# Kernel optimization log

Hardware: AMD Instinct MI355X
Metric: run time of the kernel (lower is better)

Reference implementation:

```python
import jax, jax.numpy as jnp
import numpy as np
from jax import lax

NUM_HEADS = 8
HEAD_DIM = 32  # filters_per_head


def conv1d_same(x, w, b):
    # x: [B, T, Cin], w: [K, Cin, Cout] (WIO), 'same' padding, stride 1
    y = lax.conv_general_dilated(x, w, window_strides=(1,), padding='SAME',
                                 dimension_numbers=('NWC', 'WIO', 'NWC'))
    return y + b


def setup_inputs() -> dict:
    key = jax.random.key(0)
    ks = jax.random.split(key, 9)
    B, T, C = 8, 2048, 256
    K = 3
    s = 1.0 / np.sqrt(K * C)
    return {
        'x': jax.random.normal(ks[0], (B, T, C), dtype=jnp.float32),
        'Wq': jax.random.normal(ks[1], (K, C, C), dtype=jnp.float32) * s,
        'bq': jnp.zeros((C,), dtype=jnp.float32),
        'Wk': jax.random.normal(ks[2], (K, C, C), dtype=jnp.float32) * s,
        'bk': jnp.zeros((C,), dtype=jnp.float32),
        'Wv': jax.random.normal(ks[3], (K, C, C), dtype=jnp.float32) * s,
        'bv': jnp.zeros((C,), dtype=jnp.float32),
        'Wo': jax.random.normal(ks[4], (K, C, C), dtype=jnp.float32) * s,
        'bo': jnp.zeros((C,), dtype=jnp.float32),
    }


def reference(x, Wq, bq, Wk, bk, Wv, bv, Wo, bo):
    B, T, C = x.shape
    q = conv1d_same(x, Wq, bq)
    k = conv1d_same(x, Wk, bk)
    v = conv1d_same(x, Wv, bv)

    def split(t):  # [B, T, C] -> [B, H, T, D]
        return t.reshape(B, T, NUM_HEADS, HEAD_DIM).transpose(0, 2, 1, 3)

    q, k, v = split(q), split(k), split(v)
    scale = 1.0 / jnp.sqrt(jnp.float32(HEAD_DIM))
    logits = jnp.einsum('bhqd,bhkd->bhqk', q, k) * scale  # [B,H,T,T]
    attn = jax.nn.softmax(logits, axis=-1)
    ctx = jnp.einsum('bhqk,bhkd->bhqd', attn, v)
    ctx = ctx.transpose(0, 2, 1, 3).reshape(B, T, C)
    out = x + conv1d_same(ctx, Wo, bo)
    return out
```

## Files before the change

### kernel.cpp

```cpp
#include <hip/hip_runtime.h>
#include <math.h>

#define BDIM 8
#define TDIM 2048
#define CDIM 256
#define HDIM 8
#define DDIM 32
#define TP   (TDIM + 2)

typedef __attribute__((ext_vector_type(8))) short bf16x8;
typedef __attribute__((ext_vector_type(4))) float f32x4;

#if __has_builtin(__builtin_amdgcn_exp2f)
#define EXP2(x) __builtin_amdgcn_exp2f(x)
#else
#define EXP2(x) exp2f(x)
#endif

__device__ __forceinline__ unsigned pk2(float lo, float hi) {
    union { float f; unsigned u; } a, b;
    a.f = lo; b.f = hi;
    return __builtin_amdgcn_perm(b.u + 0x8000u, a.u + 0x8000u, 0x07060302u);
}
__device__ __forceinline__ unsigned pk2t(float lo, float hi) {
    union { float f; unsigned u; } a, b;
    a.f = lo; b.f = hi;
    return __builtin_amdgcn_perm(b.u, a.u, 0x07060302u);
}
__device__ __forceinline__ short bf1(float v) {
    union { float f; unsigned u; } a; a.f = v;
    return (short)((a.u + 0x8000u) >> 16);
}
__device__ __forceinline__ void gld16(const short* g, short* l) {
    __builtin_amdgcn_global_load_lds((const __attribute__((address_space(1))) void*)g,
                                     (__attribute__((address_space(3))) void*)l, 16, 0, 0);
}

#define XBLK 832
#define WBLK 192

__global__ __launch_bounds__(256) void prep_kernel(
    const float* __restrict__ x,
    const float* __restrict__ Wq, const float* __restrict__ Wk,
    const float* __restrict__ Wv, const float* __restrict__ Wo,
    short* __restrict__ xbfp, short* __restrict__ cp,
    short* __restrict__ wcat, short* __restrict__ wot)
{
    const int tid = threadIdx.x;
    if (blockIdx.x < XBLK) {
        const int NX = BDIM * TDIM * 64;
        const int NH = 4096;
        unsigned* xw = (unsigned*)xbfp;
        unsigned* cw = (unsigned*)cp;
        for (int i = blockIdx.x * 256 + tid; i < NX + NH; i += XBLK * 256) {
            if (i < NX) {
                const int bt = i >> 6, c4 = i & 63;
                const int b = bt >> 11, t = bt & 2047;
                const float4 f = *(const float4*)(x + (size_t)bt * 256 + c4 * 4);
                const size_t wo_ = (size_t)(b * TP + t + 1) * 128 + c4 * 2;
                xw[wo_]     = pk2(f.x, f.y);
                xw[wo_ + 1] = pk2(f.z, f.w);
            } else {
                const int hz = i - NX;
                const int half = hz >> 11, z = hz & 2047;
                const int b = z >> 8, r = (z >> 7) & 1, wofs = z & 127;
                const size_t w_ = ((size_t)b * TP + (size_t)r * (TP - 1)) * 128 + wofs;
                if (half == 0) xw[w_] = 0u; else cw[w_] = 0u;
            }
        }
    } else {
        __shared__ float xs[64][65];
        const int wb = blockIdx.x - XBLK;
        const int pair = wb >> 4, sub = wb & 15;
        const int dt = pair >> 2, mat = pair & 3;
        const int ci0 = (sub >> 2) * 64, co0 = (sub & 3) * 64;
        const float* W = mat == 0 ? Wq : mat == 1 ? Wk : mat == 2 ? Wv : Wo;
        const float* src = W + dt * 65536 + (size_t)ci0 * 256 + co0;
        for (int idx = tid; idx < 4096; idx += 256) {
            const int r = idx >> 6, c = idx & 63;
            xs[r][c] = src[(size_t)r * 256 + c];
        }
        __syncthreads();
        short* dstbase = (mat < 3) ? (wcat + (size_t)(mat * 256 + co0) * 768)
                                   : (wot + (size_t)co0 * 768);
        for (int idx = tid; idx < 512; idx += 256) {
            const int co_l = idx >> 3, ci_l = (idx & 7) * 8;
            uint4 u;
            u.x = pk2(xs[ci_l + 0][co_l], xs[ci_l + 1][co_l]);
            u.y = pk2(xs[ci_l + 2][co_l], xs[ci_l + 3][co_l]);
            u.z = pk2(xs[ci_l + 4][co_l], xs[ci_l + 5][co_l]);
            u.w = pk2(xs[ci_l + 6][co_l], xs[ci_l + 7][co_l]);
            *(uint4*)(dstbase + (size_t)co_l * 768 + dt * 256 + ci0 + ci_l) = u;
        }
    }
}

__global__ __launch_bounds__(256) void gemm_qkv(
    const short* __restrict__ xbfp, const short* __restrict__ wcat,
    const float* __restrict__ bq, const float* __restrict__ bk,
    const float* __restrict__ bv,
    short* __restrict__ qo, short* __restrict__ ko, short* __restrict__ vt2)
{
    __shared__ short As[2][4096];
    __shared__ short Bs[2][4096];
    const int tid = threadIdx.x;
    const int wv = tid >> 6, lane = tid & 63, quad = lane >> 4, col = lane & 15;
    const int bx = blockIdx.x;
    const int b = bx >> 4, t0 = (bx & 15) * 128;
    const int by = blockIdx.y;
    const int qkv = by >> 1;
    const int m0 = by * 128;

    const short* wA = wcat + (size_t)m0 * 768;
    const short* xB = xbfp + ((size_t)b * TP + t0) * CDIM;
    const int r0 = tid >> 2, s0 = (tid & 3) * 8;

#define STAGE_Q(kk, bsel) do {                                                  \
    const int dt_ = (kk) >> 3, ci0_ = ((kk) & 7) * 32, k0_ = (kk) * 32;         \
    gld16(wA + (size_t)r0 * 768 + k0_ + s0,        &As[bsel][tid * 8]);         \
    gld16(wA + (size_t)(r0 + 64) * 768 + k0_ + s0, &As[bsel][tid * 8 + 2048]);  \
    gld16(xB + (size_t)(r0 + dt_) * 256 + ci0_ + s0,      &Bs[bsel][tid * 8]);  \
    gld16(xB + (size_t)(r0 + 64 + dt_) * 256 + ci0_ + s0, &Bs[bsel][tid * 8 + 2048]); \
} while (0)

    STAGE_Q(0, 0);

    const float* bias = qkv == 0 ? bq : qkv == 1 ? bk : bv;
    f32x4 acc[4][4];
#pragma unroll
    for (int mt = 0; mt < 4; ++mt) {
        const int cb = ((m0 + (wv & 1) * 64 + mt * 16) & 255) + quad * 4;
        const float4 b4 = *(const float4*)(bias + cb);
#pragma unroll
        for (int nt = 0; nt < 4; ++nt) acc[mt][nt] = (f32x4){b4.x, b4.y, b4.z, b4.w};
    }

    int bsel = 0;
    for (int kk = 0; kk < 24; ++kk) {
        __syncthreads();
        if (kk < 23) STAGE_Q(kk + 1, bsel ^ 1);
        const short* Ab = &As[bsel][((wv & 1) * 64 + col) * 32 + quad * 8];
        const short* Bb = &Bs[bsel][((wv >> 1) * 64 + col) * 32 + quad * 8];
        bf16x8 af[4], bfr[4];
#pragma unroll
        for (int i = 0; i < 4; ++i) {
            af[i]  = *(const bf16x8*)(Ab + i * 512);
            bfr[i] = *(const bf16x8*)(Bb + i * 512);
        }
#pragma unroll
        for (int mt = 0; mt < 4; ++mt)
#pragma unroll
            for (int nt = 0; nt < 4; ++nt)
                acc[mt][nt] = __builtin_amdgcn_mfma_f32_16x16x32_bf16(af[mt], bfr[nt], acc[mt][nt], 0, 0, 0);
        bsel ^= 1;
    }

    const float qs = 0.25503000508221157f;
#pragma unroll
    for (int mt = 0; mt < 4; ++mt) {
        const int cocat = m0 + (wv & 1) * 64 + mt * 16 + quad * 4;
        const int co = cocat & 255;
        const int hh = co >> 5, d = co & 31;
        const size_t bh = (size_t)b * HDIM + hh;
#pragma unroll
        for (int nt = 0; nt < 4; ++nt) {
            const int t = t0 + (wv >> 1) * 64 + nt * 16 + col;
            const f32x4 a = acc[mt][nt];
            if (qkv == 0) {
                uint2 u = make_uint2(pk2(a[0] * qs, a[1] * qs), pk2(a[2] * qs, a[3] * qs));
                *(uint2*)(qo + (bh * TDIM + t) * DDIM + d) = u;
            } else if (qkv == 1) {
                uint2 u = make_uint2(pk2(a[0], a[1]), pk2(a[2], a[3]));
                *(uint2*)(ko + (bh * TDIM + t) * DDIM + d) = u;
            } else {
                const int kt = t >> 6, u6 = t & 63, kg = u6 >> 5, rr = u6 & 31;
                const int j = ((rr >> 4) << 2) | (rr & 3), qd = (rr >> 2) & 3;
                short* vb2 = vt2 + ((bh * 32 + kt) * 2 + kg) * 1024 + qd * 8 + j;
#pragma unroll
                for (int r = 0; r < 4; ++r) vb2[(d + r) * 32] = bf1(a[r]);
            }
        }
    }
#undef STAGE_Q
}

__global__ __launch_bounds__(256) void gemm_res(
    const short* __restrict__ cp, const short* __restrict__ wot,
    const float* __restrict__ bo, const float* __restrict__ x,
    float* __restrict__ out)
{
    __shared__ short As[2][4096];
    __shared__ short Bs[2][4096];
    const int tid = threadIdx.x;
    const int wv = tid >> 6, lane = tid & 63, quad = lane >> 4, col = lane & 15;
    const int bx = blockIdx.x;
    const int b = bx >> 4, t0 = (bx & 15) * 128;
    const int m0 = blockIdx.y * 128;

    const short* wA = wot + (size_t)m0 * 768;
    const short* cB = cp + ((size_t)b * TP + t0) * CDIM;
    const int r0 = tid >> 2, s0 = (tid & 3) * 8;

#define STAGE_R(kk, bsel) do {                                                  \
    const int dt_ = (kk) >> 3, ci0_ = ((kk) & 7) * 32, k0_ = (kk) * 32;         \
    gld16(wA + (size_t)r0 * 768 + k0_ + s0,        &As[bsel][tid * 8]);         \
    gld16(wA + (size_t)(r0 + 64) * 768 + k0_ + s0, &As[bsel][tid * 8 + 2048]);  \
    gld16(cB + (size_t)(r0 + dt_) * 256 + ci0_ + s0,      &Bs[bsel][tid * 8]);  \
    gld16(cB + (size_t)(r0 + 64 + dt_) * 256 + ci0_ + s0, &Bs[bsel][tid * 8 + 2048]); \
} while (0)

    STAGE_R(0, 0);

    f32x4 acc[4][4];
#pragma unroll
    for (int mt = 0; mt < 4; ++mt) {
        const int cb = m0 + (wv & 1) * 64 + mt * 16 + quad * 4;
        const float4 b4 = *(const float4*)(bo + cb);
#pragma unroll
        for (int nt = 0; nt < 4; ++nt) acc[mt][nt] = (f32x4){b4.x, b4.y, b4.z, b4.w};
    }

    int bsel = 0;
    for (int kk = 0; kk < 24; ++kk) {
        __syncthreads();
        if (kk < 23) STAGE_R(kk + 1, bsel ^ 1);
        const short* Ab = &As[bsel][((wv & 1) * 64 + col) * 32 + quad * 8];
        const short* Bb = &Bs[bsel][((wv >> 1) * 64 + col) * 32 + quad * 8];
        bf16x8 af[4], bfr[4];
#pragma unroll
        for (int i = 0; i < 4; ++i) {
            af[i]  = *(const bf16x8*)(Ab + i * 512);
            bfr[i] = *(const bf16x8*)(Bb + i * 512);
        }
#pragma unroll
        for (int mt = 0; mt < 4; ++mt)
#pragma unroll
            for (int nt = 0; nt < 4; ++nt)
                acc[mt][nt] = __builtin_amdgcn_mfma_f32_16x16x32_bf16(af[mt], bfr[nt], acc[mt][nt], 0, 0, 0);
        bsel ^= 1;
    }

#pragma unroll
    for (int mt = 0; mt < 4; ++mt) {
        const int co = m0 + (wv & 1) * 64 + mt * 16 + quad * 4;
#pragma unroll
        for (int nt = 0; nt < 4; ++nt) {
            const int t = t0 + (wv >> 1) * 64 + nt * 16 + col;
            const size_t o = ((size_t)b * TDIM + t) * CDIM + co;
            const float4 xv = *(const float4*)(x + o);
            const f32x4 a = acc[mt][nt];
            *(float4*)(out + o) = make_float4(a[0] + xv.x, a[1] + xv.y, a[2] + xv.z, a[3] + xv.w);
        }
    }
#undef STAGE_R
}

__global__ __launch_bounds__(256, 4) void attn_kernel(
    const short* __restrict__ q, const short* __restrict__ k,
    const short* __restrict__ vt2, short* __restrict__ cp)
{
    const int tid = threadIdx.x;
    const int wv = tid >> 6, lane = tid & 63, quad = lane >> 4, col = lane & 15;
    const int bh = blockIdx.x;
    const int q0 = blockIdx.y * 128 + wv * 32;

    const short* qb = q + (size_t)bh * TDIM * DDIM;
    const short* kb = k + (size_t)bh * TDIM * DDIM;
    const short* vb = vt2 + (size_t)bh * TDIM * DDIM;

    bf16x8 qf[2];
    qf[0] = *(const bf16x8*)(qb + (size_t)(q0 + col) * DDIM + quad * 8);
    qf[1] = *(const bf16x8*)(qb + (size_t)(q0 + 16 + col) * DDIM + quad * 8);

    f32x4 acc0[2] = {{0.f,0.f,0.f,0.f},{0.f,0.f,0.f,0.f}};
    f32x4 acc1[2] = {{0.f,0.f,0.f,0.f},{0.f,0.f,0.f,0.f}};
    f32x4 accl[2] = {{0.f,0.f,0.f,0.f},{0.f,0.f,0.f,0.f}};
    const f32x4 zero = {0.f, 0.f, 0.f, 0.f};
    const short one_bf = (short)0x3F80;
    const bf16x8 ones = {one_bf, one_bf, one_bf, one_bf, one_bf, one_bf, one_bf, one_bf};

    bf16x8 kc[2][4], vf[2][4];
    const int koff = (size_t)col * 32 + quad * 8;
    const int voff = (size_t)col * 32 + quad * 8;
#pragma unroll
    for (int g = 0; g < 4; ++g) {
        kc[0][g] = *(const bf16x8*)(kb + (size_t)(g * 16) * 32 + koff);
        vf[0][g] = *(const bf16x8*)(vb + g * 512 + voff);
    }

#pragma unroll 2
    for (int kt = 0; kt < TDIM / 64; ++kt) {
        const int cur = kt & 1, nxt = cur ^ 1;
        if (kt < TDIM / 64 - 1) {
            const short* kbn = kb + (size_t)(kt + 1) * 2048;
            const short* vbn = vb + (size_t)(kt + 1) * 2048;
#pragma unroll
            for (int g = 0; g < 4; ++g) {
                kc[nxt][g] = *(const bf16x8*)(kbn + (size_t)(g * 16) * 32 + koff);
                vf[nxt][g] = *(const bf16x8*)(vbn + g * 512 + voff);
            }
        }
#pragma unroll
        for (int qi = 0; qi < 2; ++qi) {
            f32x4 s[4];
#pragma unroll
            for (int g = 0; g < 4; ++g)
                s[g] = __builtin_amdgcn_mfma_f32_16x16x32_bf16(kc[cur][g], qf[qi], zero, 0, 0, 0);
            float p[16];
#pragma unroll
            for (int g = 0; g < 4; ++g)
#pragma unroll
                for (int r = 0; r < 4; ++r)
                    p[g * 4 + r] = EXP2(s[g][r]);
            union { unsigned u[4]; bf16x8 v; } P0, P1;
            P0.u[0] = pk2t(p[0], p[1]);   P0.u[1] = pk2t(p[2], p[3]);
            P0.u[2] = pk2t(p[4], p[5]);   P0.u[3] = pk2t(p[6], p[7]);
            P1.u[0] = pk2t(p[8], p[9]);   P1.u[1] = pk2t(p[10], p[11]);
            P1.u[2] = pk2t(p[12], p[13]); P1.u[3] = pk2t(p[14], p[15]);
            acc0[qi] = __builtin_amdgcn_mfma_f32_16x16x32_bf16(vf[cur][0], P0.v, acc0[qi], 0, 0, 0);
            acc1[qi] = __builtin_amdgcn_mfma_f32_16x16x32_bf16(vf[cur][1], P0.v, acc1[qi], 0, 0, 0);
            accl[qi] = __builtin_amdgcn_mfma_f32_16x16x32_bf16(ones,       P0.v, accl[qi], 0, 0, 0);
            acc0[qi] = __builtin_amdgcn_mfma_f32_16x16x32_bf16(vf[cur][2], P1.v, acc0[qi], 0, 0, 0);
            acc1[qi] = __builtin_amdgcn_mfma_f32_16x16x32_bf16(vf[cur][3], P1.v, acc1[qi], 0, 0, 0);
            accl[qi] = __builtin_amdgcn_mfma_f32_16x16x32_bf16(ones,       P1.v, accl[qi], 0, 0, 0);
        }
    }

    const int b = bh >> 3, hh = bh & 7;
#pragma unroll
    for (int qi = 0; qi < 2; ++qi) {
        const float inv = 1.f / accl[qi][0];
        const int t = q0 + qi * 16 + col;
        short* crow = cp + ((size_t)b * TP + t + 1) * CDIM + hh * DDIM;
        uint2 u0 = make_uint2(pk2(acc0[qi][0] * inv, acc0[qi][1] * inv),
                              pk2(acc0[qi][2] * inv, acc0[qi][3] * inv));
        uint2 u1 = make_uint2(pk2(acc1[qi][0] * inv, acc1[qi][1] * inv),
                              pk2(acc1[qi][2] * inv, acc1[qi][3] * inv));
        *(uint2*)(crow + quad * 4)      = u0;
        *(uint2*)(crow + 16 + quad * 4) = u1;
    }
}

extern "C" void kernel_launch(void* const* d_in, const int* in_sizes, int n_in,
                              void* d_out, int out_size, void* d_ws, size_t ws_size,
                              hipStream_t stream) {
    const float* x  = (const float*)d_in[0];
    const float* Wq = (const float*)d_in[1];
    const float* bq = (const float*)d_in[2];
    const float* Wk = (const float*)d_in[3];
    const float* bk = (const float*)d_in[4];
    const float* Wv = (const float*)d_in[5];
    const float* bv = (const float*)d_in[6];
    const float* Wo = (const float*)d_in[7];
    const float* bo = (const float*)d_in[8];
    float* out = (float*)d_out;

    short* p = (short*)d_ws;
    short* xbfp = p; p += (size_t)BDIM * TP * CDIM;
    short* cpb  = p; p += (size_t)BDIM * TP * CDIM;
    short* qbuf = p; p += (size_t)BDIM * HDIM * TDIM * DDIM;
    short* kbuf = p; p += (size_t)BDIM * HDIM * TDIM * DDIM;
    short* vt2  = p; p += (size_t)BDIM * HDIM * TDIM * DDIM;
    short* wcat = p; p += 768 * 768;
    short* wot  = p; p += 256 * 768;

    prep_kernel<<<dim3(XBLK + WBLK), 256, 0, stream>>>(x, Wq, Wk, Wv, Wo, xbfp, cpb, wcat, wot);
    gemm_qkv<<<dim3(128, 6), 256, 0, stream>>>(xbfp, wcat, bq, bk, bv, qbuf, kbuf, vt2);
    attn_kernel<<<dim3(64, 16), 256, 0, stream>>>(qbuf, kbuf, vt2, cpb);
    gemm_res<<<dim3(128, 2), 256, 0, stream>>>(cpb, wot, bo, x, out);
}
```

Before: 203.2 us.

## Stage K/V tiles through double-buffered LDS shared by all waves

Each block now loads each 64-key K and V tile cooperatively into shared memory once, with each thread fetching one 16-byte chunk. The loads are double-buffered, with the next tile's global read issued before compute and stored to LDS afterwards. Waves then read their MFMA fragments from LDS instead of each wave loading the whole tile from global memory. This cuts redundant global/L2 traffic by a factor of four, at the cost of a __syncthreads per tile and extra LDS reads.

```diff
diff --git a/kernel.cpp b/kernel.cpp
--- a/kernel.cpp
+++ b/kernel.cpp
@@ -259,6 +259,8 @@
     const short* __restrict__ q, const short* __restrict__ k,
     const short* __restrict__ vt2, short* __restrict__ cp)
 {
+    __shared__ short ks[2][2048];
+    __shared__ short vs[2][2048];
     const int tid = threadIdx.x;
     const int wv = tid >> 6, lane = tid & 63, quad = lane >> 4, col = lane & 15;
     const int bh = blockIdx.x;
@@ -267,6 +269,14 @@
     const short* qb = q + (size_t)bh * TDIM * DDIM;
     const short* kb = k + (size_t)bh * TDIM * DDIM;
     const short* vb = vt2 + (size_t)bh * TDIM * DDIM;
+    const int so = tid * 8;
+
+    {
+        uint4 kr = *(const uint4*)(kb + so);
+        uint4 vr = *(const uint4*)(vb + so);
+        *(uint4*)&ks[0][so] = kr;
+        *(uint4*)&vs[0][so] = vr;
+    }
 
     bf16x8 qf[2];
     qf[0] = *(const bf16x8*)(qb + (size_t)(q0 + col) * DDIM + quad * 8);
@@ -279,33 +289,30 @@
     const short one_bf = (short)0x3F80;
     const bf16x8 ones = {one_bf, one_bf, one_bf, one_bf, one_bf, one_bf, one_bf, one_bf};
 
-    bf16x8 kc[2][4], vf[2][4];
-    const int koff = (size_t)col * 32 + quad * 8;
-    const int voff = (size_t)col * 32 + quad * 8;
-#pragma unroll
-    for (int g = 0; g < 4; ++g) {
-        kc[0][g] = *(const bf16x8*)(kb + (size_t)(g * 16) * 32 + koff);
-        vf[0][g] = *(const bf16x8*)(vb + g * 512 + voff);
-    }
+    const int foff = col * 32 + quad * 8;
+    __syncthreads();
 
 #pragma unroll 2
     for (int kt = 0; kt < TDIM / 64; ++kt) {
-        const int cur = kt & 1, nxt = cur ^ 1;
-        if (kt < TDIM / 64 - 1) {
-            const short* kbn = kb + (size_t)(kt + 1) * 2048;
-            const short* vbn = vb + (size_t)(kt + 1) * 2048;
-#pragma unroll
-            for (int g = 0; g < 4; ++g) {
-                kc[nxt][g] = *(const bf16x8*)(kbn + (size_t)(g * 16) * 32 + koff);
-                vf[nxt][g] = *(const bf16x8*)(vbn + g * 512 + voff);
-            }
+        const int cur = kt & 1;
+        uint4 krn, vrn;
+        const bool more = kt < TDIM / 64 - 1;
+        if (more) {
+            krn = *(const uint4*)(kb + (kt + 1) * 2048 + so);
+            vrn = *(const uint4*)(vb + (kt + 1) * 2048 + so);
+        }
+        bf16x8 kc[4], vf[4];
+#pragma unroll
+        for (int g = 0; g < 4; ++g) {
+            kc[g] = *(const bf16x8*)&ks[cur][g * 512 + foff];
+            vf[g] = *(const bf16x8*)&vs[cur][g * 512 + foff];
         }
 #pragma unroll
         for (int qi = 0; qi < 2; ++qi) {
             f32x4 s[4];
 #pragma unroll
             for (int g = 0; g < 4; ++g)
-                s[g] = __builtin_amdgcn_mfma_f32_16x16x32_bf16(kc[cur][g], qf[qi], zero, 0, 0, 0);
+                s[g] = __builtin_amdgcn_mfma_f32_16x16x32_bf16(kc[g], qf[qi], zero, 0, 0, 0);
             float p[16];
 #pragma unroll
             for (int g = 0; g < 4; ++g)
@@ -317,13 +324,18 @@
             P0.u[2] = pk2t(p[4], p[5]);   P0.u[3] = pk2t(p[6], p[7]);
             P1.u[0] = pk2t(p[8], p[9]);   P1.u[1] = pk2t(p[10], p[11]);
             P1.u[2] = pk2t(p[12], p[13]); P1.u[3] = pk2t(p[14], p[15]);
-            acc0[qi] = __builtin_amdgcn_mfma_f32_16x16x32_bf16(vf[cur][0], P0.v, acc0[qi], 0, 0, 0);
-            acc1[qi] = __builtin_amdgcn_mfma_f32_16x16x32_bf16(vf[cur][1], P0.v, acc1[qi], 0, 0, 0);
-            accl[qi] = __builtin_amdgcn_mfma_f32_16x16x32_bf16(ones,       P0.v, accl[qi], 0, 0, 0);
-            acc0[qi] = __builtin_amdgcn_mfma_f32_16x16x32_bf16(vf[cur][2], P1.v, acc0[qi], 0, 0, 0);
-            acc1[qi] = __builtin_amdgcn_mfma_f32_16x16x32_bf16(vf[cur][3], P1.v, acc1[qi], 0, 0, 0);
-            accl[qi] = __builtin_amdgcn_mfma_f32_16x16x32_bf16(ones,       P1.v, accl[qi], 0, 0, 0);
-        }
+            acc0[qi] = __builtin_amdgcn_mfma_f32_16x16x32_bf16(vf[0], P0.v, acc0[qi], 0, 0, 0);
+            acc1[qi] = __builtin_amdgcn_mfma_f32_16x16x32_bf16(vf[1], P0.v, acc1[qi], 0, 0, 0);
+            accl[qi] = __builtin_amdgcn_mfma_f32_16x16x32_bf16(ones,  P0.v, accl[qi], 0, 0, 0);
+            acc0[qi] = __builtin_amdgcn_mfma_f32_16x16x32_bf16(vf[2], P1.v, acc0[qi], 0, 0, 0);
+            acc1[qi] = __builtin_amdgcn_mfma_f32_16x16x32_bf16(vf[3], P1.v, acc1[qi], 0, 0, 0);
+            accl[qi] = __builtin_amdgcn_mfma_f32_16x16x32_bf16(ones,  P1.v, accl[qi], 0, 0, 0);
+        }
+        if (more) {
+            *(uint4*)&ks[cur ^ 1][so] = krn;
+            *(uint4*)&vs[cur ^ 1][so] = vrn;
+        }
+        __syncthreads();
     }
 
     const int b = bh >> 3, hh = bh & 7;
```

Result: faster. 185.5 us (-8.7%).
